# Performance work log

Measured on AMD Instinct MI355X. Metric: run time of the kernel, lower is better.

Reference implementation:

```python
import jax, jax.numpy as jnp
import numpy as np

# Module hyperparameters (init_kwargs)
OSFREQ = 8.0
MAXFREQ = 1.0
SP = 1.0
THRESH = 0.0

B, C, T = 8, 64, 1200


def _periodogram_cfg(n_samples):
    # Mirrors hypercoil's _periodogram_cfg
    timespan = SP * (n_samples + 1) - 1
    all_samples = np.arange(SP, timespan + 1, SP)
    freqstep = 1.0 / (timespan * OSFREQ)
    angular_frequencies = 2.0 * np.pi * np.arange(
        freqstep, MAXFREQ * n_samples / (2.0 * timespan) + freqstep, freqstep
    )
    return (
        jnp.asarray(angular_frequencies, jnp.float32),  # [K]
        jnp.asarray(all_samples, jnp.float32),          # [T]
    )


def setup_inputs() -> dict:
    key = jax.random.key(0)
    k1, k2 = jax.random.split(key)
    data = jax.random.normal(k1, (B, C, T), dtype=jnp.float32)
    mask = jax.random.randint(k2, (B, T), 0, 2).astype(bool)
    return {"input": data, "mask": mask}


def _fit_spectrum(basis, m, dm):
    # basis: [B,K,T] shifted trig basis; m: [B,T] mask weights; dm: [B,C,T] masked data
    num = jnp.einsum('bkt,bct->bkc', basis, dm)              # masked projection
    denom = jnp.einsum('bkt,bkt,bt->bk', basis, basis, m)    # masked basis norm
    coef = num / denom[..., None]
    if THRESH > 0:
        a = jnp.abs(coef)
        coef = jnp.where(a / a.max() > THRESH, coef, 0.0)
    return coef


def spectral_interpolate(data, mask):
    omega, t = _periodogram_cfg(data.shape[-1])  # [K], [T]
    m = mask.astype(data.dtype)                  # [B,T]
    arg2 = 2.0 * omega[:, None] * t[None, :]     # [K,T]
    # Lomb-Scargle time offsets tau per (batch, frequency), over observed samples only
    tau = jnp.arctan2(
        jnp.einsum('bt,kt->bk', m, jnp.sin(arg2)),
        jnp.einsum('bt,kt->bk', m, jnp.cos(arg2)),
    ) / (2.0 * omega)[None, :]                   # [B,K]
    theta = omega[None, :, None] * (t[None, None, :] - tau[:, :, None])  # [B,K,T]
    cosb = jnp.cos(theta)
    sinb = jnp.sin(theta)
    dm = data * m[:, None, :]                    # masked (degraded) data [B,C,T]
    c_coef = _fit_spectrum(cosb, m, dm)          # [B,K,C]
    s_coef = _fit_spectrum(sinb, m, dm)
    recon = (jnp.einsum('bkt,bkc->bct', cosb, c_coef)
             + jnp.einsum('bkt,bkc->bct', sinb, s_coef))      # [B,C,T]
    # Normalise: match std of reconstruction to std of observed data
    std_recon = jnp.std(recon, axis=-1, ddof=1, keepdims=True)
    cnt = m.sum(-1)[:, None, None]
    mu = dm.sum(-1, keepdims=True) / cnt
    var = ((data - mu) ** 2 * m[:, None, :]).sum(-1, keepdims=True) / (cnt - 1.0)
    std_orig = jnp.sqrt(var)
    recon = recon * (std_orig / std_recon)
    # Keep observed samples; fill censored samples with reconstruction
    return jnp.where(mask[:, None, :], data, recon)


def reference(input, mask):
    return spectral_interpolate(input, mask)
```

## Files before the change

### kernel.cpp

```cpp
#include <hip/hip_runtime.h>
#include <math.h>

#define B_ 8
#define C_ 64
#define M_ 512
#define T_ 1200
#define TP2 1280
#define KP 4864
#define K2P 9728
#define SPLITK 8
#define KCH 1216
#define NST1 20
#define NST2 19
#define TCH 152

#ifndef M_PI
#define M_PI 3.14159265358979323846
#endif

typedef _Float16 h8 __attribute__((ext_vector_type(8)));
typedef float f32x16 __attribute__((ext_vector_type(16)));
union H8 { h8 h; float4 v; _Float16 e[8]; };
union HP { _Float16 hh[2]; unsigned u; };
union F4U { float4 v; float f[4]; };

#define Z16v {0.f,0.f,0.f,0.f,0.f,0.f,0.f,0.f,0.f,0.f,0.f,0.f,0.f,0.f,0.f,0.f}
#define MFMA32(a, b, c) __builtin_amdgcn_mfma_f32_32x32x16_f16(a, b, c, 0, 0, 0)

__device__ __forceinline__ float2 cmul(float2 a, float2 b) {
    return make_float2(a.x * b.x - a.y * b.y, a.y * b.x + a.x * b.y);
}

__device__ __forceinline__ void gload16(const void* g, void* l) {
    __builtin_amdgcn_global_load_lds(
        (const __attribute__((address_space(1))) unsigned int*)g,
        (__attribute__((address_space(3))) unsigned int*)l, 16, 0, 0);
}

__device__ int detect_mode(const void* mask_raw) {
    __shared__ int sb0, sb1;
    if (threadIdx.x == 0) { sb0 = 0; sb1 = 0; }
    __syncthreads();
    const unsigned* wi = (const unsigned*)mask_raw;
    const float* wf = (const float*)mask_raw;
    int nw = (B_ * T_) >> 2;
    int badI = 0, badF = 0;
    for (int i = threadIdx.x; i < nw; i += blockDim.x) {
        unsigned v = wi[i];
        badI |= (v > 1u);
        float f = wf[i];
        badF |= !(f == 0.0f || f == 1.0f);
    }
    if (badI) sb0 = 1;
    if (badF) sb1 = 1;
    __syncthreads();
    return (!sb0) ? 0 : ((!sb1) ? 1 : 2);
}

__device__ __forceinline__ float mval(const void* mask_raw, int mode, int idx) {
    if (mode == 0) return (float)((const int*)mask_raw)[idx];
    if (mode == 1) return ((const float*)mask_raw)[idx];
    return (float)((const unsigned char*)mask_raw)[idx];
}

__device__ __forceinline__ double omega_w(int k, double fstep) {
    double om = 2.0 * M_PI * (fstep + (double)k * fstep);
    return (double)((float)om);
}

__global__ __launch_bounds__(256) void prep3_kernel(
    const float* __restrict__ data, const void* __restrict__ mask,
    float* __restrict__ cnt,
    _Float16* __restrict__ dm, float* __restrict__ partS, float* __restrict__ partC,
    _Float16* __restrict__ Zb, _Float16* __restrict__ ZT, int K, double fstep) {
    __shared__ float mfS[B_][TCH];
    __shared__ _Float16 sZ[128 * 80];
    __shared__ _Float16 sZT[64 * 136];
    __shared__ float2 rotS[4][64];
    int bx = blockIdx.x, tid = threadIdx.x;
    if (bx < 320) {
        int mode = detect_mode(mask);
        int base = (bx * 256 + tid) * 8;
        int t = base % TP2, bc = base / TP2;
        H8 o;
        if (t < T_) {
            int b = bc >> 6;
            F4U d0, d1;
            d0.v = *(const float4*)&data[bc * T_ + t];
            d1.v = *(const float4*)&data[bc * T_ + t + 4];
#pragma unroll
            for (int e = 0; e < 4; e++) {
                o.e[e]     = (_Float16)(d0.f[e] * mval(mask, mode, b * T_ + t + e));
                o.e[e + 4] = (_Float16)(d1.f[e] * mval(mask, mode, b * T_ + t + 4 + e));
            }
        } else {
#pragma unroll
            for (int e = 0; e < 8; e++) o.e[e] = (_Float16)0.f;
        }
        *(float4*)&dm[base] = o.v;
        return;
    }
    if (bx < 472) {
        int mode = detect_mode(mask);
        int i0 = bx - 320;
        int kb = i0 % 19, chunk = i0 / 19;
        for (int i = tid; i < B_ * TCH; i += 256) {
            int b = i / TCH, tt = i % TCH;
            int t = chunk * TCH + tt;
            mfS[b][tt] = (t < T_) ? mval(mask, mode, b * T_ + t) : 0.f;
        }
        __syncthreads();
        int k = kb * 256 + tid;
        double w = omega_w(k, fstep);
        double ds, dc;
        sincos(2.0 * w, &ds, &dc);
        float2 r2 = make_float2((float)dc, (float)ds);
        sincos(304.0 * w, &ds, &dc);
        float2 r304 = make_float2((float)dc, (float)ds);
        float2 r = r2;
        {
            int e = chunk;
            float2 p = r304;
            while (e) { if (e & 1) r = cmul(r, p); p = cmul(p, p); e >>= 1; }
        }
        float s2a[B_], c2a[B_];
#pragma unroll
        for (int b = 0; b < B_; b++) { s2a[b] = 0.f; c2a[b] = 0.f; }
        for (int tt = 0; tt < TCH; tt++) {
            float sv = r.y, cv = r.x;
#pragma unroll
            for (int b = 0; b < B_; b++) {
                float m = mfS[b][tt];
                s2a[b] = fmaf(m, sv, s2a[b]);
                c2a[b] = fmaf(m, cv, c2a[b]);
            }
            r = cmul(r, r2);
        }
#pragma unroll
        for (int b = 0; b < B_; b++) {
            partS[(size_t)(chunk * 8 + b) * KP + k] = s2a[b];
            partC[(size_t)(chunk * 8 + b) * KP + k] = c2a[b];
        }
        return;
    }
    if (bx < 1992) {
        int i0 = bx - 472;
        int kb = i0 / 20, tb = i0 % 20;
        int k0 = kb * 64, t0 = tb * 64;
        int kk = tid >> 2, tq = tid & 3;
        {
            double w = omega_w(k0 + kk, fstep);
            double mult = (tq == 0) ? 1.0 : (tq == 1) ? 8.0 : (tq == 2) ? 32.0 : 64.0;
            double ds, dc;
            sincos(mult * w, &ds, &dc);
            rotS[tq][kk] = make_float2((float)dc, (float)ds);
        }
        __syncthreads();
        int k = k0 + kk;
        float2 r1 = rotS[0][kk];
        float2 acc = r1;
        {
            float2 p = rotS[1][kk];
            if (tq & 1) acc = cmul(acc, p);
            p = cmul(p, p);
            if (tq & 2) acc = cmul(acc, p);
        }
        {
            int e = tb;
            float2 p = rotS[3][kk];
            while (e) { if (e & 1) acc = cmul(acc, p); p = cmul(p, p); e >>= 1; }
        }
        bool kv = (k < K);
        float2 r32 = rotS[2][kk];
#pragma unroll
        for (int j = 0; j < 2; j++) {
            float2 r = acc;
            H8 hc, hs;
#pragma unroll
            for (int d = 0; d < 8; d++) {
                int tl = tq * 8 + j * 32 + d;
                bool ok = kv && (t0 + tl < T_);
                float c = ok ? r.x : 0.f, s = ok ? r.y : 0.f;
                hc.e[d] = (_Float16)c; hs.e[d] = (_Float16)s;
                HP pk; pk.hh[0] = hc.e[d]; pk.hh[1] = hs.e[d];
                *(unsigned*)&sZT[tl * 136 + 2 * kk] = pk.u;
                r = cmul(r, r1);
            }
            int ch = tq + 4 * j;
            int rc = 2 * kk, rs = 2 * kk + 1;
            *(float4*)&sZ[rc * 80 + ((ch ^ (rc & 7)) << 3)] = hc.v;
            *(float4*)&sZ[rs * 80 + ((ch ^ (rs & 7)) << 3)] = hs.v;
            acc = cmul(acc, r32);
        }
        __syncthreads();
        {
            int c8 = tid & 7, rr = tid >> 3;
#pragma unroll
            for (int p = 0; p < 4; p++) {
                int row = p * 32 + rr;
                float4 v = *(const float4*)&sZ[row * 80 + ((c8 ^ (row & 7)) << 3)];
                *(float4*)&Zb[(size_t)(2 * k0 + row) * TP2 + t0 + c8 * 8] = v;
            }
        }
        {
            int c16 = tid & 15, rr = tid >> 4;
#pragma unroll
            for (int p = 0; p < 4; p++) {
                int row = p * 16 + rr;
                float4 v = *(const float4*)&sZT[row * 136 + c16 * 8];
                *(float4*)&ZT[(size_t)(t0 + row) * K2P + 2 * k0 + c16 * 8] = v;
            }
        }
        return;
    }
    {
        int mode = detect_mode(mask);
        __shared__ float red[256];
        for (int b = 0; b < B_; b++) {
            float s = 0.f;
            for (int t = tid; t < T_; t += 256) s += mval(mask, mode, b * T_ + t);
            red[tid] = s; __syncthreads();
            for (int w = 128; w > 0; w >>= 1) {
                if (tid < w) red[tid] += red[tid + w];
                __syncthreads();
            }
            if (tid == 0) cnt[b] = red[0];
            __syncthreads();
        }
    }
}

__global__ __launch_bounds__(256, 3) void gemm1x(
    const _Float16* __restrict__ dm, const _Float16* __restrict__ Zb,
    const float* __restrict__ partS, const float* __restrict__ partC,
    const float* __restrict__ cnt,
    _Float16* __restrict__ Wout) {
    __shared__ _Float16 lds[24576];
    char* ldsb = (char*)lds;
    int bx = blockIdx.x;
    int g = (bx & 7) * 76 + (bx >> 3);
    int mt = g & 7, nt = g >> 3;
    int m0 = mt * 64, n0 = nt * 128;
    int tid = threadIdx.x, lane = tid & 63, wv = tid >> 6;
    int ra = lane & 31, kg = lane >> 5, x = ra & 7;
    int wm = (wv & 1) * 32, wn = (wv >> 1) * 64;
    int r0 = wm + ra, q0 = wn + ra;
    f32x16 acc0 = Z16v, acc1 = Z16v;
    int sAo[2], sBo[4];
#pragma unroll
    for (int i = 0; i < 2; i++) {
        int g8 = i * 256 + tid;
        int r = g8 >> 3, c = g8 & 7;
        sAo[i] = r * 2560 + ((c ^ (r & 7)) << 4);
    }
#pragma unroll
    for (int i = 0; i < 4; i++) {
        int g8 = i * 256 + tid;
        int r = g8 >> 3, c = g8 & 7;
        sBo[i] = r * 2560 + ((c ^ (r & 7)) << 4);
    }
    const char* pA = (const char*)dm + (size_t)m0 * 2560;
    const char* pB = (const char*)Zb + (size_t)n0 * 2560;
#define STG1(BUFOFF, RC) do {                                                  \
        char* Ld_ = ldsb + (BUFOFF);                                           \
        _Pragma("unroll")                                                      \
        for (int i_ = 0; i_ < 2; i_++)                                         \
            gload16(pA + (RC) + sAo[i_], Ld_ + ((i_ * 256 + tid) << 4));       \
        _Pragma("unroll")                                                      \
        for (int i_ = 0; i_ < 4; i_++)                                         \
            gload16(pB + (RC) + sBo[i_], Ld_ + 8192 + ((i_ * 256 + tid) << 4));\
    } while (0)
    STG1(0, 0);
    __syncthreads();
    int cur = 0;
    for (int step = 0; step < NST1; step++) {
        if (step + 1 < NST1) STG1((cur ^ 1) * 24576, (step + 1) << 7);
        const char* LA = ldsb + cur * 24576;
        const char* LB = LA + 8192;
#pragma unroll
        for (int kc = 0; kc < 4; kc++) {
            int c = kc * 2 + kg;
            h8 a0 = *(const h8*)(LA + ((r0 * 8 + (c ^ x)) << 4));
            h8 b0 = *(const h8*)(LB + ((q0 * 8 + (c ^ x)) << 4));
            h8 b1 = *(const h8*)(LB + (((q0 + 32) * 8 + (c ^ x)) << 4));
            acc0 = MFMA32(a0, b0, acc0);
            acc1 = MFMA32(a0, b1, acc1);
        }
        __syncthreads();
        cur ^= 1;
    }
#undef STG1
    int bb = mt;
    int colk = lane & 31, rb4 = (lane >> 5) * 4;
    float cn = cnt[bb];
    float cpJ[2], spJ[2], rcJ[2], rsJ[2];
#pragma unroll
    for (int J = 0; J < 2; J++) {
        int k2 = n0 + wn + 32 * J + colk;
        int k = k2 >> 1;
        float s2 = 0.f, c2 = 0.f;
#pragma unroll
        for (int c = 0; c < 8; c++) {
            s2 += partS[(size_t)(c * 8 + bb) * KP + k];
            c2 += partC[(size_t)(c * 8 + bb) * KP + k];
        }
        float phi = 0.5f * atan2f(s2, c2);
        float cp = cosf(phi), sp = sinf(phi);
        float A = 0.5f * (cn + c2), D = 0.5f * (cn - c2), E = 0.5f * s2;
        cpJ[J] = cp; spJ[J] = sp;
        rcJ[J] = 1.f / (cp * cp * A + 2.f * cp * sp * E + sp * sp * D);
        rsJ[J] = 1.f / (sp * sp * A - 2.f * cp * sp * E + cp * cp * D);
    }
#define EPI1(ACC, J) {                                                         \
        int k2 = n0 + wn + 32 * (J) + colk;                                    \
        float cp = cpJ[J], sp = spJ[J];                                        \
        float rc_ = rcJ[J], rs_ = rsJ[J];                                      \
        int par = k2 & 1;                                                      \
        _Pragma("unroll")                                                      \
        for (int reg = 0; reg < 16; reg++) {                                   \
            float own = (ACC)[reg];                                            \
            float oth = __shfl_xor(own, 1);                                    \
            float p = par ? oth : own, q = par ? own : oth;                    \
            float cc = (cp * p + sp * q) * rc_;                                \
            float sc = (cp * q - sp * p) * rs_;                                \
            float val = par ? (sp * cc + cp * sc) : (cp * cc - sp * sc);       \
            int row = m0 + wm + rb4 + (reg & 3) + 8 * (reg >> 2);              \
            Wout[(size_t)row * K2P + k2] = (_Float16)val;                      \
        } }
    EPI1(acc0, 0); EPI1(acc1, 1);
#undef EPI1
}

__global__ __launch_bounds__(256, 3) void gemm2x(
    const _Float16* __restrict__ Wm, const _Float16* __restrict__ ZT,
    _Float16* __restrict__ rpart) {
    __shared__ _Float16 lds[24576];
    char* ldsb = (char*)lds;
    int bx = blockIdx.x;
    int sk = bx & 7;
    int g2 = bx >> 3;
    int mt = g2 & 3, tt = g2 >> 2;
    int m0 = mt * 128, t0 = tt * 64;
    int tid = threadIdx.x, lane = tid & 63, wv = tid >> 6;
    int ra = lane & 31, kg = lane >> 5, x = ra & 7;
    int wm = (wv & 1) * 64, wn = (wv >> 1) * 32;
    int r0 = wm + ra, q0 = wn + ra;
    f32x16 acc0 = Z16v, acc1 = Z16v;
    int sAo[4], sBo[2];
#pragma unroll
    for (int i = 0; i < 4; i++) {
        int g8 = i * 256 + tid;
        int r = g8 >> 3, c = g8 & 7;
        sAo[i] = r * 19456 + ((c ^ (r & 7)) << 4);
    }
#pragma unroll
    for (int i = 0; i < 2; i++) {
        int g8 = i * 256 + tid;
        int r = g8 >> 3, c = g8 & 7;
        sBo[i] = r * 19456 + ((c ^ (r & 7)) << 4);
    }
    const char* pA = (const char*)Wm + (size_t)m0 * 19456 + sk * 2432;
    const char* pB = (const char*)ZT + (size_t)t0 * 19456 + sk * 2432;
#define STG2(BUFOFF, RC) do {                                                  \
        char* Ld_ = ldsb + (BUFOFF);                                           \
        _Pragma("unroll")                                                      \
        for (int i_ = 0; i_ < 4; i_++)                                         \
            gload16(pA + (RC) + sAo[i_], Ld_ + ((i_ * 256 + tid) << 4));       \
        _Pragma("unroll")                                                      \
        for (int i_ = 0; i_ < 2; i_++)                                         \
            gload16(pB + (RC) + sBo[i_], Ld_ + 16384 + ((i_ * 256 + tid) << 4));\
    } while (0)
    STG2(0, 0);
    __syncthreads();
    int cur = 0;
    for (int step = 0; step < NST2; step++) {
        if (step + 1 < NST2) STG2((cur ^ 1) * 24576, (step + 1) << 7);
        const char* LA = ldsb + cur * 24576;
        const char* LB = LA + 16384;
#pragma unroll
        for (int kc = 0; kc < 4; kc++) {
            int c = kc * 2 + kg;
            h8 a0 = *(const h8*)(LA + ((r0 * 8 + (c ^ x)) << 4));
            h8 a1 = *(const h8*)(LA + (((r0 + 32) * 8 + (c ^ x)) << 4));
            h8 b0 = *(const h8*)(LB + ((q0 * 8 + (c ^ x)) << 4));
            acc0 = MFMA32(a0, b0, acc0);
            acc1 = MFMA32(a1, b0, acc1);
        }
        __syncthreads();
        cur ^= 1;
    }
#undef STG2
    int colk = lane & 31, rb4 = (lane >> 5) * 4;
    int t = t0 + wn + colk;
#define EPI2(ACC, I) {                                                         \
        _Pragma("unroll")                                                      \
        for (int reg = 0; reg < 16; reg++) {                                   \
            int row = m0 + wm + 32 * (I) + rb4 + (reg & 3) + 8 * (reg >> 2);   \
            rpart[(size_t)(sk * M_ + row) * TP2 + t] = (_Float16)(ACC)[reg];   \
        } }
    EPI2(acc0, 0); EPI2(acc1, 1);
#undef EPI2
}

__global__ __launch_bounds__(256) void norm3_kernel(
    const _Float16* __restrict__ rpart, const float* __restrict__ data,
    const void* __restrict__ mask, const float* __restrict__ cnt,
    float* __restrict__ out) {
    int mode = detect_mode(mask);
    __shared__ float rsum[T_];
    __shared__ float4 red4[256];
    __shared__ float s_scale;
    int bc = blockIdx.x, b = bc >> 6;
    const size_t rbase = (size_t)bc * TP2;
    const size_t dbase = (size_t)bc * T_;
    const size_t rstr = (size_t)M_ * TP2;
    float sr = 0.f, srr = 0.f, sd = 0.f, sdd = 0.f;
    for (int t = threadIdx.x; t < T_; t += 256) {
        float r = 0.f;
#pragma unroll
        for (int s = 0; s < SPLITK; s++) r += (float)rpart[s * rstr + rbase + t];
        rsum[t] = r;
        float m = mval(mask, mode, b * T_ + t);
        float xv = data[dbase + t];
        sr += r; srr += r * r; sd += xv * m; sdd += xv * xv * m;
    }
    red4[threadIdx.x] = make_float4(sr, srr, sd, sdd);
    __syncthreads();
    for (int w = 128; w > 0; w >>= 1) {
        if (threadIdx.x < w) {
            float4 a = red4[threadIdx.x], c = red4[threadIdx.x + w];
            red4[threadIdx.x] = make_float4(a.x + c.x, a.y + c.y, a.z + c.z, a.w + c.w);
        }
        __syncthreads();
    }
    if (threadIdx.x == 0) {
        float4 v = red4[0];
        float cn = cnt[b];
        float varr = (v.y - v.x * v.x / (float)T_) / (float)(T_ - 1);
        float vard = (v.w - v.z * v.z / cn) / (cn - 1.f);
        s_scale = sqrtf(vard / varr);
    }
    __syncthreads();
    float scale = s_scale;
    for (int t = threadIdx.x; t < T_; t += 256) {
        float m = mval(mask, mode, b * T_ + t);
        out[dbase + t] = (m > 0.5f) ? data[dbase + t] : rsum[t] * scale;
    }
}

extern "C" void kernel_launch(void* const* d_in, const int* in_sizes, int n_in,
                              void* d_out, int out_size, void* d_ws, size_t ws_size,
                              hipStream_t stream) {
    const float* data = (const float*)d_in[0];
    const void* mask = d_in[1];
    float* out = (float*)d_out;

    const double timespan = 1.0 * (T_ + 1) - 1.0;
    const double fstep = 1.0 / (timespan * 8.0);
    const double stop = (1.0 * (double)T_) / (2.0 * timespan) + fstep;
    const int K = (int)ceil((stop - fstep) / fstep);

    char* w = (char*)d_ws;
    auto alloc = [&](size_t nbytes) {
        char* p = w;
        w += ((nbytes + 255) / 256) * 256;
        return p;
    };
    float*     cnt   = (float*)    alloc(B_ * 4);
    float*     partS = (float*)    alloc((size_t)64 * KP * 4);
    float*     partC = (float*)    alloc((size_t)64 * KP * 4);
    _Float16*  dm_h  = (_Float16*) alloc((size_t)M_ * TP2 * 2);
    _Float16*  Z     = (_Float16*) alloc((size_t)K2P * TP2 * 2);
    _Float16*  ZT    = (_Float16*) alloc((size_t)TP2 * K2P * 2);
    _Float16*  W     = (_Float16*) alloc((size_t)M_ * K2P * 2);
    _Float16*  rpart = (_Float16*) alloc((size_t)SPLITK * M_ * TP2 * 2);
    (void)ws_size; (void)in_sizes; (void)n_in; (void)out_size;

    prep3_kernel<<<1993, 256, 0, stream>>>(data, mask, cnt, dm_h, partS, partC,
                                           Z, ZT, K, fstep);
    gemm1x<<<608, 256, 0, stream>>>(dm_h, Z, partS, partC, cnt, W);
    gemm2x<<<640, 256, 0, stream>>>(W, ZT, rpart);
    norm3_kernel<<<M_, 256, 0, stream>>>(rpart, data, mask, cnt, out);
}
```

Measured before the change: 90.91 us.

## Generate trig basis on the fly inside GEMMs instead of materializing Z/ZT

Removes the prep-stage blocks that wrote the fp16 cosine/sine basis Z and its transpose ZT to global memory. The basis tiles are now computed directly into LDS inside gemm1x and gemm2x by complex rotation recurrences seeded with double-precision sincos. This cuts about 50 MB of global writes and reads plus a large block of prep work. It also vectorises the mask loads in the dm prep path. The cost is extra ALU and LDS-store work in each GEMM pipeline step, and possible fp16 precision drift from long rotation chains.

Measured after the change: 92.09 us. About the same (+1.3%).

```diff
diff --git a/kernel.cpp b/kernel.cpp
--- a/kernel.cpp
+++ b/kernel.cpp
@@ -21,7 +21,6 @@
 typedef _Float16 h8 __attribute__((ext_vector_type(8)));
 typedef float f32x16 __attribute__((ext_vector_type(16)));
 union H8 { h8 h; float4 v; _Float16 e[8]; };
-union HP { _Float16 hh[2]; unsigned u; };
 union F4U { float4 v; float f[4]; };
 
 #define Z16v {0.f,0.f,0.f,0.f,0.f,0.f,0.f,0.f,0.f,0.f,0.f,0.f,0.f,0.f,0.f,0.f}
@@ -68,30 +67,48 @@
     return (double)((float)om);
 }
 
-__global__ __launch_bounds__(256) void prep3_kernel(
+__global__ __launch_bounds__(256) void prep4_kernel(
     const float* __restrict__ data, const void* __restrict__ mask,
     float* __restrict__ cnt,
     _Float16* __restrict__ dm, float* __restrict__ partS, float* __restrict__ partC,
-    _Float16* __restrict__ Zb, _Float16* __restrict__ ZT, int K, double fstep) {
+    double fstep) {
     __shared__ float mfS[B_][TCH];
-    __shared__ _Float16 sZ[128 * 80];
-    __shared__ _Float16 sZT[64 * 136];
-    __shared__ float2 rotS[4][64];
     int bx = blockIdx.x, tid = threadIdx.x;
+    int mode = detect_mode(mask);
     if (bx < 320) {
-        int mode = detect_mode(mask);
         int base = (bx * 256 + tid) * 8;
         int t = base % TP2, bc = base / TP2;
         H8 o;
         if (t < T_) {
             int b = bc >> 6;
+            int mi = b * T_ + t;
+            float mv[8];
+            if (mode == 0) {
+                int4 v0 = *(const int4*)((const int*)mask + mi);
+                int4 v1 = *(const int4*)((const int*)mask + mi + 4);
+                mv[0] = (float)v0.x; mv[1] = (float)v0.y; mv[2] = (float)v0.z; mv[3] = (float)v0.w;
+                mv[4] = (float)v1.x; mv[5] = (float)v1.y; mv[6] = (float)v1.z; mv[7] = (float)v1.w;
+            } else if (mode == 1) {
+                F4U a0, a1;
+                a0.v = *(const float4*)((const float*)mask + mi);
+                a1.v = *(const float4*)((const float*)mask + mi + 4);
+#pragma unroll
+                for (int e = 0; e < 4; e++) { mv[e] = a0.f[e]; mv[e + 4] = a1.f[e]; }
+            } else {
+                uint2 u = *(const uint2*)((const unsigned char*)mask + mi);
+#pragma unroll
+                for (int e = 0; e < 4; e++) {
+                    mv[e]     = (float)((u.x >> (8 * e)) & 0xff);
+                    mv[e + 4] = (float)((u.y >> (8 * e)) & 0xff);
+                }
+            }
             F4U d0, d1;
             d0.v = *(const float4*)&data[bc * T_ + t];
             d1.v = *(const float4*)&data[bc * T_ + t + 4];
 #pragma unroll
             for (int e = 0; e < 4; e++) {
-                o.e[e]     = (_Float16)(d0.f[e] * mval(mask, mode, b * T_ + t + e));
-                o.e[e + 4] = (_Float16)(d1.f[e] * mval(mask, mode, b * T_ + t + 4 + e));
+                o.e[e]     = (_Float16)(d0.f[e] * mv[e]);
+                o.e[e + 4] = (_Float16)(d1.f[e] * mv[e + 4]);
             }
         } else {
 #pragma unroll
@@ -101,7 +118,6 @@
         return;
     }
     if (bx < 472) {
-        int mode = detect_mode(mask);
         int i0 = bx - 320;
         int kb = i0 % 19, chunk = i0 / 19;
         for (int i = tid; i < B_ * TCH; i += 256) {
@@ -143,78 +159,7 @@
         }
         return;
     }
-    if (bx < 1992) {
-        int i0 = bx - 472;
-        int kb = i0 / 20, tb = i0 % 20;
-        int k0 = kb * 64, t0 = tb * 64;
-        int kk = tid >> 2, tq = tid & 3;
-        {
-            double w = omega_w(k0 + kk, fstep);
-            double mult = (tq == 0) ? 1.0 : (tq == 1) ? 8.0 : (tq == 2) ? 32.0 : 64.0;
-            double ds, dc;
-            sincos(mult * w, &ds, &dc);
-            rotS[tq][kk] = make_float2((float)dc, (float)ds);
-        }
-        __syncthreads();
-        int k = k0 + kk;
-        float2 r1 = rotS[0][kk];
-        float2 acc = r1;
-        {
-            float2 p = rotS[1][kk];
-            if (tq & 1) acc = cmul(acc, p);
-            p = cmul(p, p);
-            if (tq & 2) acc = cmul(acc, p);
-        }
-        {
-            int e = tb;
-            float2 p = rotS[3][kk];
-            while (e) { if (e & 1) acc = cmul(acc, p); p = cmul(p, p); e >>= 1; }
-        }
-        bool kv = (k < K);
-        float2 r32 = rotS[2][kk];
-#pragma unroll
-        for (int j = 0; j < 2; j++) {
-            float2 r = acc;
-            H8 hc, hs;
-#pragma unroll
-            for (int d = 0; d < 8; d++) {
-                int tl = tq * 8 + j * 32 + d;
-                bool ok = kv && (t0 + tl < T_);
-                float c = ok ? r.x : 0.f, s = ok ? r.y : 0.f;
-                hc.e[d] = (_Float16)c; hs.e[d] = (_Float16)s;
-                HP pk; pk.hh[0] = hc.e[d]; pk.hh[1] = hs.e[d];
-                *(unsigned*)&sZT[tl * 136 + 2 * kk] = pk.u;
-                r = cmul(r, r1);
-            }
-            int ch = tq + 4 * j;
-            int rc = 2 * kk, rs = 2 * kk + 1;
-            *(float4*)&sZ[rc * 80 + ((ch ^ (rc & 7)) << 3)] = hc.v;
-            *(float4*)&sZ[rs * 80 + ((ch ^ (rs & 7)) << 3)] = hs.v;
-            acc = cmul(acc, r32);
-        }
-        __syncthreads();
-        {
-            int c8 = tid & 7, rr = tid >> 3;
-#pragma unroll
-            for (int p = 0; p < 4; p++) {
-                int row = p * 32 + rr;
-                float4 v = *(const float4*)&sZ[row * 80 + ((c8 ^ (row & 7)) << 3)];
-                *(float4*)&Zb[(size_t)(2 * k0 + row) * TP2 + t0 + c8 * 8] = v;
-            }
-        }
-        {
-            int c16 = tid & 15, rr = tid >> 4;
-#pragma unroll
-            for (int p = 0; p < 4; p++) {
-                int row = p * 16 + rr;
-                float4 v = *(const float4*)&sZT[row * 136 + c16 * 8];
-                *(float4*)&ZT[(size_t)(t0 + row) * K2P + 2 * k0 + c16 * 8] = v;
-            }
-        }
-        return;
-    }
     {
-        int mode = detect_mode(mask);
         __shared__ float red[256];
         for (int b = 0; b < B_; b++) {
             float s = 0.f;
@@ -231,10 +176,10 @@
 }
 
 __global__ __launch_bounds__(256, 3) void gemm1x(
-    const _Float16* __restrict__ dm, const _Float16* __restrict__ Zb,
+    const _Float16* __restrict__ dm,
     const float* __restrict__ partS, const float* __restrict__ partC,
     const float* __restrict__ cnt,
-    _Float16* __restrict__ Wout) {
+    _Float16* __restrict__ Wout, double fstep) {
     __shared__ _Float16 lds[24576];
     char* ldsb = (char*)lds;
     int bx = blockIdx.x;
@@ -246,35 +191,60 @@
     int wm = (wv & 1) * 32, wn = (wv >> 1) * 64;
     int r0 = wm + ra, q0 = wn + ra;
     f32x16 acc0 = Z16v, acc1 = Z16v;
-    int sAo[2], sBo[4];
+    int kk = tid >> 2, tq = tid & 3;
+    double wth = omega_w((n0 >> 1) + kk, fstep);
+    double sd_, cd_;
+    sincos(wth * (double)(tq * 16 + 1), &sd_, &cd_);
+    float2 pth = make_float2((float)cd_, (float)sd_);
+    sincos(wth, &sd_, &cd_);
+    float2 r1th = make_float2((float)cd_, (float)sd_);
+    float2 r64th = r1th;
+#pragma unroll
+    for (int i = 0; i < 6; i++) r64th = cmul(r64th, r64th);
+    int sAo[2];
 #pragma unroll
     for (int i = 0; i < 2; i++) {
         int g8 = i * 256 + tid;
         int r = g8 >> 3, c = g8 & 7;
         sAo[i] = r * 2560 + ((c ^ (r & 7)) << 4);
     }
-#pragma unroll
-    for (int i = 0; i < 4; i++) {
-        int g8 = i * 256 + tid;
-        int r = g8 >> 3, c = g8 & 7;
-        sBo[i] = r * 2560 + ((c ^ (r & 7)) << 4);
-    }
     const char* pA = (const char*)dm + (size_t)m0 * 2560;
-    const char* pB = (const char*)Zb + (size_t)n0 * 2560;
-#define STG1(BUFOFF, RC) do {                                                  \
+#define STG1A(BUFOFF, RC) do {                                                 \
         char* Ld_ = ldsb + (BUFOFF);                                           \
         _Pragma("unroll")                                                      \
         for (int i_ = 0; i_ < 2; i_++)                                         \
             gload16(pA + (RC) + sAo[i_], Ld_ + ((i_ * 256 + tid) << 4));       \
-        _Pragma("unroll")                                                      \
-        for (int i_ = 0; i_ < 4; i_++)                                         \
-            gload16(pB + (RC) + sBo[i_], Ld_ + 8192 + ((i_ * 256 + tid) << 4));\
     } while (0)
-    STG1(0, 0);
+#define GEN1(BUFOFF) do {                                                      \
+        char* Bd_ = ldsb + (BUFOFF) + 8192;                                    \
+        float2 q_ = pth;                                                       \
+        H8 c0_, c1_, s0_, s1_;                                                 \
+        _Pragma("unroll")                                                      \
+        for (int j_ = 0; j_ < 8; j_++) {                                       \
+            c0_.e[j_] = (_Float16)q_.x; s0_.e[j_] = (_Float16)q_.y;            \
+            q_ = cmul(q_, r1th);                                               \
+        }                                                                      \
+        _Pragma("unroll")                                                      \
+        for (int j_ = 0; j_ < 8; j_++) {                                       \
+            c1_.e[j_] = (_Float16)q_.x; s1_.e[j_] = (_Float16)q_.y;            \
+            q_ = cmul(q_, r1th);                                               \
+        }                                                                      \
+        int rc_ = 2 * kk, rs_ = rc_ + 1;                                       \
+        *(float4*)(Bd_ + ((rc_ * 8 + ((tq * 2)     ^ (rc_ & 7))) << 4)) = c0_.v; \
+        *(float4*)(Bd_ + ((rc_ * 8 + ((tq * 2 + 1) ^ (rc_ & 7))) << 4)) = c1_.v; \
+        *(float4*)(Bd_ + ((rs_ * 8 + ((tq * 2)     ^ (rs_ & 7))) << 4)) = s0_.v; \
+        *(float4*)(Bd_ + ((rs_ * 8 + ((tq * 2 + 1) ^ (rs_ & 7))) << 4)) = s1_.v; \
+        pth = cmul(pth, r64th);                                                \
+    } while (0)
+    STG1A(0, 0);
+    GEN1(0);
     __syncthreads();
     int cur = 0;
     for (int step = 0; step < NST1; step++) {
-        if (step + 1 < NST1) STG1((cur ^ 1) * 24576, (step + 1) << 7);
+        if (step + 1 < NST1) {
+            STG1A((cur ^ 1) * 24576, (step + 1) << 7);
+            GEN1((cur ^ 1) * 24576);
+        }
         const char* LA = ldsb + cur * 24576;
         const char* LB = LA + 8192;
 #pragma unroll
@@ -289,7 +259,8 @@
         __syncthreads();
         cur ^= 1;
     }
-#undef STG1
+#undef STG1A
+#undef GEN1
     int bb = mt;
     int colk = lane & 31, rb4 = (lane >> 5) * 4;
     float cn = cnt[bb];
@@ -332,8 +303,8 @@
 }
 
 __global__ __launch_bounds__(256, 3) void gemm2x(
-    const _Float16* __restrict__ Wm, const _Float16* __restrict__ ZT,
-    _Float16* __restrict__ rpart) {
+    const _Float16* __restrict__ Wm,
+    _Float16* __restrict__ rpart, int K, double fstep) {
     __shared__ _Float16 lds[24576];
     char* ldsb = (char*)lds;
     int bx = blockIdx.x;
@@ -346,35 +317,65 @@
     int wm = (wv & 1) * 64, wn = (wv >> 1) * 32;
     int r0 = wm + ra, q0 = wn + ra;
     f32x16 acc0 = Z16v, acc1 = Z16v;
-    int sAo[4], sBo[2];
+    int rt = tid >> 2, kq = tid & 3;
+    int tp1 = t0 + rt + 1;
+    int kth0 = sk * 608 + kq * 8;
+    double w0 = omega_w(kth0, fstep);
+    double sd_, cd_;
+    sincos(w0 * (double)tp1, &sd_, &cd_);
+    float2 pth = make_float2((float)cd_, (float)sd_);
+    double s1d = 2.0 * M_PI * fstep * (double)tp1;
+    sincos(s1d, &sd_, &cd_);
+    float2 dlt = make_float2((float)cd_, (float)sd_);
+    float2 d32 = dlt;
+#pragma unroll
+    for (int i = 0; i < 5; i++) d32 = cmul(d32, d32);
+    int sAo[4];
 #pragma unroll
     for (int i = 0; i < 4; i++) {
         int g8 = i * 256 + tid;
         int r = g8 >> 3, c = g8 & 7;
         sAo[i] = r * 19456 + ((c ^ (r & 7)) << 4);
     }
-#pragma unroll
-    for (int i = 0; i < 2; i++) {
-        int g8 = i * 256 + tid;
-        int r = g8 >> 3, c = g8 & 7;
-        sBo[i] = r * 19456 + ((c ^ (r & 7)) << 4);
-    }
     const char* pA = (const char*)Wm + (size_t)m0 * 19456 + sk * 2432;
-    const char* pB = (const char*)ZT + (size_t)t0 * 19456 + sk * 2432;
-#define STG2(BUFOFF, RC) do {                                                  \
+#define STG2A(BUFOFF, RC) do {                                                 \
         char* Ld_ = ldsb + (BUFOFF);                                           \
         _Pragma("unroll")                                                      \
         for (int i_ = 0; i_ < 4; i_++)                                         \
             gload16(pA + (RC) + sAo[i_], Ld_ + ((i_ * 256 + tid) << 4));       \
-        _Pragma("unroll")                                                      \
-        for (int i_ = 0; i_ < 2; i_++)                                         \
-            gload16(pB + (RC) + sBo[i_], Ld_ + 16384 + ((i_ * 256 + tid) << 4));\
     } while (0)
-    STG2(0, 0);
+#define GEN2(BUFOFF, STEP) do {                                                \
+        char* Bd_ = ldsb + (BUFOFF) + 16384;                                   \
+        float2 q_ = pth;                                                       \
+        int kc_ = kth0 + (STEP) * 32;                                          \
+        H8 h0_, h1_;                                                           \
+        _Pragma("unroll")                                                      \
+        for (int j_ = 0; j_ < 4; j_++) {                                       \
+            bool ok_ = (kc_ + j_) < K;                                         \
+            h0_.e[2 * j_]     = (_Float16)(ok_ ? q_.x : 0.f);                  \
+            h0_.e[2 * j_ + 1] = (_Float16)(ok_ ? q_.y : 0.f);                  \
+            q_ = cmul(q_, dlt);                                                \
+        }                                                                      \
+        _Pragma("unroll")                                                      \
+        for (int j_ = 0; j_ < 4; j_++) {                                       \
+            bool ok_ = (kc_ + 4 + j_) < K;                                     \
+            h1_.e[2 * j_]     = (_Float16)(ok_ ? q_.x : 0.f);                  \
+            h1_.e[2 * j_ + 1] = (_Float16)(ok_ ? q_.y : 0.f);                  \
+            q_ = cmul(q_, dlt);                                                \
+        }                                                                      \
+        *(float4*)(Bd_ + ((rt * 8 + ((kq * 2)     ^ (rt & 7))) << 4)) = h0_.v; \
+        *(float4*)(Bd_ + ((rt * 8 + ((kq * 2 + 1) ^ (rt & 7))) << 4)) = h1_.v; \
+        pth = cmul(pth, d32);                                                  \
+    } while (0)
+    STG2A(0, 0);
+    GEN2(0, 0);
     __syncthreads();
     int cur = 0;
     for (int step = 0; step < NST2; step++) {
-        if (step + 1 < NST2) STG2((cur ^ 1) * 24576, (step + 1) << 7);
+        if (step + 1 < NST2) {
+            STG2A((cur ^ 1) * 24576, (step + 1) << 7);
+            GEN2((cur ^ 1) * 24576, step + 1);
+        }
         const char* LA = ldsb + cur * 24576;
         const char* LB = LA + 16384;
 #pragma unroll
@@ -389,7 +390,8 @@
         __syncthreads();
         cur ^= 1;
     }
-#undef STG2
+#undef STG2A
+#undef GEN2
     int colk = lane & 31, rb4 = (lane >> 5) * 4;
     int t = t0 + wn + colk;
 #define EPI2(ACC, I) {                                                         \
@@ -470,15 +472,12 @@
     float*     partS = (float*)    alloc((size_t)64 * KP * 4);
     float*     partC = (float*)    alloc((size_t)64 * KP * 4);
     _Float16*  dm_h  = (_Float16*) alloc((size_t)M_ * TP2 * 2);
-    _Float16*  Z     = (_Float16*) alloc((size_t)K2P * TP2 * 2);
-    _Float16*  ZT    = (_Float16*) alloc((size_t)TP2 * K2P * 2);
     _Float16*  W     = (_Float16*) alloc((size_t)M_ * K2P * 2);
     _Float16*  rpart = (_Float16*) alloc((size_t)SPLITK * M_ * TP2 * 2);
     (void)ws_size; (void)in_sizes; (void)n_in; (void)out_size;
 
-    prep3_kernel<<<1993, 256, 0, stream>>>(data, mask, cnt, dm_h, partS, partC,
-                                           Z, ZT, K, fstep);
-    gemm1x<<<608, 256, 0, stream>>>(dm_h, Z, partS, partC, cnt, W);
-    gemm2x<<<640, 256, 0, stream>>>(W, ZT, rpart);
+    prep4_kernel<<<473, 256, 0, stream>>>(data, mask, cnt, dm_h, partS, partC, fstep);
+    gemm1x<<<608, 256, 0, stream>>>(dm_h, partS, partC, cnt, W, fstep);
+    gemm2x<<<640, 256, 0, stream>>>(W, rpart, K, fstep);
     norm3_kernel<<<M_, 256, 0, stream>>>(rpart, data, mask, cnt, out);
 }
```
